# Kernel tuning notes

Hardware: AMD Instinct MI355X
Metric: run time of the kernel (lower is better)

The kernel has to match this reference:

```python
import jax, jax.numpy as jnp
import numpy as np

B, I, H, T = 65536, 64, 64, 16  # batch, input_size, hidden_size, type_num


def setup_inputs() -> dict:
    key = jax.random.key(0)
    ks = jax.random.split(key, 10)
    s = 0.1  # ~1/sqrt(H) init scale like torch GRUCell
    return {
        "x": jax.random.normal(ks[0], (B, I), jnp.float32),
        "typ": jax.random.randint(ks[1], (B,), 0, T, jnp.int32),
        "c": jax.random.normal(ks[2], (B, H), jnp.float32),
        "registers": jax.random.normal(ks[3], (B, T, H), jnp.float32),
        # per-type GRUCell bank (stacked across types)
        "Wih": jax.random.normal(ks[4], (T, 3 * H, I), jnp.float32) * s,
        "Whh": jax.random.normal(ks[5], (T, 3 * H, H), jnp.float32) * s,
        "bih": jax.random.normal(ks[6], (T, 3 * H), jnp.float32) * s,
        "bhh": jax.random.normal(ks[7], (T, 3 * H), jnp.float32) * s,
        # core GRUCell: input = flattened registers (T*H)
        "cWih": jax.random.normal(ks[8], (3 * H, T * H), jnp.float32) * s,
        "cWhh": jax.random.normal(ks[9], (3 * H, H), jnp.float32) * s,
        "cbih": jnp.zeros((3 * H,), jnp.float32),
        "cbhh": jnp.zeros((3 * H,), jnp.float32),
    }


def _gru(gi, gh, h):
    # torch.nn.GRUCell math; gi/gh: (..., 3H), h: (..., H)
    ir, iz, in_ = jnp.split(gi, 3, axis=-1)
    hr, hz, hn = jnp.split(gh, 3, axis=-1)
    r = jax.nn.sigmoid(ir + hr)
    z = jax.nn.sigmoid(iz + hz)
    n = jnp.tanh(in_ + r * hn)
    return (1.0 - z) * n + z * h


def reference(x, typ, c, registers, Wih, Whh, bih, bhh, cWih, cWhh, cbih, cbhh):
    # Bank of T GRUCells, all run on the same input x with per-type hidden = registers[:, t]
    gi = jnp.einsum('bi,tgi->btg', x, Wih) + bih[None]            # (B,T,3H)
    gh = jnp.einsum('bth,tgh->btg', registers, Whh) + bhh[None]   # (B,T,3H)
    hidden_tmp = _gru(gi, gh, registers)                          # (B,T,H)

    # Gather/scatter register update: only slot typ[b] takes its GRU output,
    # all other slots keep the old register (exactly what hidden_all[N, I] does).
    mask = (jnp.arange(T)[None, :] == typ[:, None])[..., None]    # (B,T,1)
    reg_new = jnp.where(mask, hidden_tmp, registers)              # (B,T,H)

    # core_v2: core GRUCell over flattened registers with state c
    xflat = reg_new.reshape(B, T * H)
    cgi = xflat @ cWih.T + cbih
    cgh = c @ cWhh.T + cbhh
    core = _gru(cgi, cgh, c)                                      # (B,H)
    return core
```

## Files before the change

kernel.cpp:

```cpp
#include <hip/hip_runtime.h>

typedef unsigned short u16;
typedef unsigned int u32;
typedef __bf16 bf16x8 __attribute__((ext_vector_type(8)));
typedef float f32x4 __attribute__((ext_vector_type(4)));
typedef u32 u32x2 __attribute__((ext_vector_type(2)));
typedef u32 u32x4 __attribute__((ext_vector_type(4)));


__device__ __forceinline__ u16 f2bf(float f) {
  union { float f; u32 u; } v; v.f = f;
  u32 u = v.u;
  u32 r = (u + 0x7fffu + ((u >> 16) & 1u)) >> 16;
  return (u16)r;
}
__device__ __forceinline__ float bf2f(u16 h) {
  union { u32 u; float f; } v; v.u = ((u32)h) << 16;
  return v.f;
}
__device__ __forceinline__ u32 pack2(float a, float b) {
  return (u32)f2bf(a) | ((u32)f2bf(b) << 16);
}
__device__ __forceinline__ float sigf(float x) { return 1.0f / (1.0f + __expf(-x)); }
__device__ __forceinline__ float tanh_fast(float x) { return 2.0f * sigf(2.0f * x) - 1.0f; }

__global__ __launch_bounds__(256) void k0_convert(
    const float* __restrict__ Wih, const float* __restrict__ Whh,
    const float* __restrict__ cWih, const float* __restrict__ cWhh,
    u16* __restrict__ wih_bf, u16* __restrict__ whh_bf,
    u16* __restrict__ cwih_bf, u16* __restrict__ cwhh_bf)
{
  int i = blockIdx.x * 256 + threadIdx.x;
  if (i < 196608) {
    wih_bf[i]  = f2bf(Wih[i]);
    whh_bf[i]  = f2bf(Whh[i]);
    cwih_bf[i] = f2bf(cWih[i]);
  }
  if (i < 12288) cwhh_bf[i] = f2bf(cWhh[i]);
}

__global__ __launch_bounds__(256) void k1_pertype(
    const float* __restrict__ x, const int* __restrict__ typ,
    const float* __restrict__ regs,
    const u16* __restrict__ wih_bf, const u16* __restrict__ whh_bf,
    const float* __restrict__ bih, const float* __restrict__ bhh,
    u16* __restrict__ hnew)
{
  const int t = blockIdx.y;
  const int base = blockIdx.x * 1024;
  const int tid = threadIdx.x;

  __shared__ int s_count;
  __shared__ int s_list[1024];
  __shared__ __align__(16) u16 sAx[16 * 72];
  __shared__ __align__(16) u16 sAh[16 * 72];

  if (tid == 0) s_count = 0;
  __syncthreads();
  for (int i = tid; i < 1024; i += 256) {
    if (typ[base + i] == t) {
      int p = atomicAdd(&s_count, 1);
      s_list[p] = base + i;
    }
  }
  __syncthreads();
  const int count = s_count;
  if (count == 0) return;

  const int lane = tid & 63;
  const int w = tid >> 6;
  const int col = lane & 15;
  const int quad = lane >> 4;
  const int hidx = w * 16 + col;

  bf16x8 bw[3][2], bh[3][2];
#pragma unroll
  for (int g = 0; g < 3; ++g) {
    const u16* pw = wih_bf + (t * 192 + g * 64 + hidx) * 64;
    const u16* ph = whh_bf + (t * 192 + g * 64 + hidx) * 64;
#pragma unroll
    for (int s = 0; s < 2; ++s) {
      bw[g][s] = *(const bf16x8*)(pw + s * 32 + quad * 8);
      bh[g][s] = *(const bf16x8*)(ph + s * 32 + quad * 8);
    }
  }
  float vbih[3], vbhh[3];
#pragma unroll
  for (int g = 0; g < 3; ++g) {
    vbih[g] = bih[t * 192 + g * 64 + hidx];
    vbhh[g] = bhh[t * 192 + g * 64 + hidx];
  }

  const int srow = tid >> 4;
  const int sk4 = (tid & 15) * 4;
  const f32x4 zero = {0.f, 0.f, 0.f, 0.f};

  for (int tile = 0; tile < count; tile += 16) {
    __syncthreads();
    {
      int r = tile + srow;
      int b = s_list[r < count ? r : count - 1];
      float4 vx = *(const float4*)(x + b * 64 + sk4);
      float4 vh = *(const float4*)(regs + (b * 16 + t) * 64 + sk4);
      u32x2 px, ph2;
      px[0] = pack2(vx.x, vx.y); px[1] = pack2(vx.z, vx.w);
      ph2[0] = pack2(vh.x, vh.y); ph2[1] = pack2(vh.z, vh.w);
      *(u32x2*)(&sAx[srow * 72 + sk4]) = px;
      *(u32x2*)(&sAh[srow * 72 + sk4]) = ph2;
    }
    __syncthreads();

    f32x4 agi[3], agh[3];
#pragma unroll
    for (int g = 0; g < 3; ++g) { agi[g] = zero; agh[g] = zero; }
#pragma unroll
    for (int s = 0; s < 2; ++s) {
      bf16x8 ax = *(const bf16x8*)(&sAx[col * 72 + s * 32 + quad * 8]);
      bf16x8 ah = *(const bf16x8*)(&sAh[col * 72 + s * 32 + quad * 8]);
#pragma unroll
      for (int g = 0; g < 3; ++g) {
        agi[g] = __builtin_amdgcn_mfma_f32_16x16x32_bf16(ax, bw[g][s], agi[g], 0, 0, 0);
        agh[g] = __builtin_amdgcn_mfma_f32_16x16x32_bf16(ah, bh[g][s], agh[g], 0, 0, 0);
      }
    }
#pragma unroll
    for (int rr = 0; rr < 4; ++rr) {
      int m = quad * 4 + rr;
      int gr = tile + m;
      if (gr < count) {
        int b2 = s_list[gr];
        float ir  = agi[0][rr] + vbih[0];
        float iz  = agi[1][rr] + vbih[1];
        float in_ = agi[2][rr] + vbih[2];
        float hr  = agh[0][rr] + vbhh[0];
        float hz  = agh[1][rr] + vbhh[1];
        float hn  = agh[2][rr] + vbhh[2];
        float rg = sigf(ir + hr);
        float zg = sigf(iz + hz);
        float ng = tanh_fast(in_ + rg * hn);
        float hold = bf2f(sAh[m * 72 + hidx]);
        hnew[b2 * 64 + hidx] = f2bf((1.f - zg) * ng + zg * hold);
      }
    }
  }
}

__global__ __launch_bounds__(256) void k2_core(
    const float* __restrict__ regs, const int* __restrict__ typ,
    const float* __restrict__ c, const u16* __restrict__ hnew,
    const u16* __restrict__ cwih_bf, const u16* __restrict__ cwhh_bf,
    const float* __restrict__ cbih, const float* __restrict__ cbhh,
    float* __restrict__ out)
{
  __shared__ __align__(16) u16 sA[64 * 72];
  __shared__ __align__(16) u16 sB[192 * 72];
  __shared__ int s_typ[64];

  const int tid = threadIdx.x;
  const int rowbase = blockIdx.x * 64;
  if (tid < 64) s_typ[tid] = typ[rowbase + tid];

  const int lane = tid & 63;
  const int w = tid >> 6;
  const int col = lane & 15;
  const int quad = lane >> 4;
  const f32x4 zero = {0.f, 0.f, 0.f, 0.f};

  f32x4 agi[4][3];
#pragma unroll
  for (int mt = 0; mt < 4; ++mt)
#pragma unroll
    for (int g = 0; g < 3; ++g) agi[mt][g] = zero;

  for (int s = 0; s < 16; ++s) {
    __syncthreads();
#pragma unroll
    for (int j = 0; j < 6; ++j) {
      int u = tid + 256 * j;
      int n = u >> 3, ko = (u & 7) * 8;
      *(u32x4*)(&sB[n * 72 + ko]) = *(const u32x4*)(cwih_bf + n * 1024 + s * 64 + ko);
    }
#pragma unroll
    for (int j = 0; j < 4; ++j) {
      int v = tid + 256 * j;
      int row = v >> 4, k4 = (v & 15) * 4;
      int b = rowbase + row;
      if (s_typ[row] == s) {
        *(u32x2*)(&sA[row * 72 + k4]) = *(const u32x2*)(hnew + b * 64 + k4);
      } else {
        float4 vv = *(const float4*)(regs + (b * 16 + s) * 64 + k4);
        u32x2 pp; pp[0] = pack2(vv.x, vv.y); pp[1] = pack2(vv.z, vv.w);
        *(u32x2*)(&sA[row * 72 + k4]) = pp;
      }
    }
    __syncthreads();
#pragma unroll
    for (int ks = 0; ks < 2; ++ks) {
      bf16x8 bfr[3];
#pragma unroll
      for (int g = 0; g < 3; ++g)
        bfr[g] = *(const bf16x8*)(&sB[(g * 64 + w * 16 + col) * 72 + ks * 32 + quad * 8]);
#pragma unroll
      for (int mt = 0; mt < 4; ++mt) {
        bf16x8 af = *(const bf16x8*)(&sA[(mt * 16 + col) * 72 + ks * 32 + quad * 8]);
#pragma unroll
        for (int g = 0; g < 3; ++g)
          agi[mt][g] = __builtin_amdgcn_mfma_f32_16x16x32_bf16(af, bfr[g], agi[mt][g], 0, 0, 0);
      }
    }
  }

  f32x4 agh[4][3];
#pragma unroll
  for (int mt = 0; mt < 4; ++mt)
#pragma unroll
    for (int g = 0; g < 3; ++g) agh[mt][g] = zero;

  __syncthreads();
#pragma unroll
  for (int j = 0; j < 6; ++j) {
    int u = tid + 256 * j;
    int n = u >> 3, ko = (u & 7) * 8;
    *(u32x4*)(&sB[n * 72 + ko]) = *(const u32x4*)(cwhh_bf + n * 64 + ko);
  }
#pragma unroll
  for (int j = 0; j < 4; ++j) {
    int v = tid + 256 * j;
    int row = v >> 4, k4 = (v & 15) * 4;
    int b = rowbase + row;
    float4 vv = *(const float4*)(c + b * 64 + k4);
    u32x2 pp; pp[0] = pack2(vv.x, vv.y); pp[1] = pack2(vv.z, vv.w);
    *(u32x2*)(&sA[row * 72 + k4]) = pp;
  }
  __syncthreads();
#pragma unroll
  for (int ks = 0; ks < 2; ++ks) {
    bf16x8 bfr[3];
#pragma unroll
    for (int g = 0; g < 3; ++g)
      bfr[g] = *(const bf16x8*)(&sB[(g * 64 + w * 16 + col) * 72 + ks * 32 + quad * 8]);
#pragma unroll
    for (int mt = 0; mt < 4; ++mt) {
      bf16x8 af = *(const bf16x8*)(&sA[(mt * 16 + col) * 72 + ks * 32 + quad * 8]);
#pragma unroll
      for (int g = 0; g < 3; ++g)
        agh[mt][g] = __builtin_amdgcn_mfma_f32_16x16x32_bf16(af, bfr[g], agh[mt][g], 0, 0, 0);
    }
  }

  const int hidx = w * 16 + col;
  float b0 = cbih[hidx], b1 = cbih[64 + hidx], b2 = cbih[128 + hidx];
  float d0 = cbhh[hidx], d1 = cbhh[64 + hidx], d2 = cbhh[128 + hidx];
#pragma unroll
  for (int mt = 0; mt < 4; ++mt) {
#pragma unroll
    for (int rr = 0; rr < 4; ++rr) {
      int row = mt * 16 + quad * 4 + rr;
      int b = rowbase + row;
      float ir  = agi[mt][0][rr] + b0;
      float iz  = agi[mt][1][rr] + b1;
      float in_ = agi[mt][2][rr] + b2;
      float hr  = agh[mt][0][rr] + d0;
      float hz  = agh[mt][1][rr] + d1;
      float hn  = agh[mt][2][rr] + d2;
      float rg = sigf(ir + hr);
      float zg = sigf(iz + hz);
      float ng = tanh_fast(in_ + rg * hn);
      float cold = c[b * 64 + hidx];
      out[b * 64 + hidx] = (1.f - zg) * ng + zg * cold;
    }
  }
}

extern "C" void kernel_launch(void* const* d_in, const int* in_sizes, int n_in,
                              void* d_out, int out_size, void* d_ws, size_t ws_size,
                              hipStream_t stream) {
  const float* x    = (const float*)d_in[0];
  const int*   typ  = (const int*)d_in[1];
  const float* c    = (const float*)d_in[2];
  const float* regs = (const float*)d_in[3];
  const float* Wih  = (const float*)d_in[4];
  const float* Whh  = (const float*)d_in[5];
  const float* bih  = (const float*)d_in[6];
  const float* bhh  = (const float*)d_in[7];
  const float* cWih = (const float*)d_in[8];
  const float* cWhh = (const float*)d_in[9];
  const float* cbih = (const float*)d_in[10];
  const float* cbhh = (const float*)d_in[11];
  float* out = (float*)d_out;

  char* ws = (char*)d_ws;
  u16* hnew    = (u16*)ws;
  u16* wih_bf  = (u16*)(ws + (size_t)8 * 1024 * 1024);
  u16* whh_bf  = wih_bf + 196608;
  u16* cwih_bf = whh_bf + 196608;
  u16* cwhh_bf = cwih_bf + 196608;

  k0_convert<<<768, 256, 0, stream>>>(Wih, Whh, cWih, cWhh, wih_bf, whh_bf, cwih_bf, cwhh_bf);
  k1_pertype<<<dim3(64, 16), 256, 0, stream>>>(x, typ, regs, wih_bf, whh_bf, bih, bhh, hnew);
  k2_core<<<1024, 256, 0, stream>>>(regs, typ, c, hnew, cwih_bf, cwhh_bf, cbih, cbhh, out);
}
```

Before: 543.8 us.

## Fuse per-type GRU and core GRU into one kernel with LDS-resident registers

Merges the per-type GRU kernel and the core GRU kernel into a single kernel. Each 64-row block loads its full register slab once into LDS as bf16, sorts rows by type, and computes the per-type GRU outputs into LDS. The core GEMM then reads from LDS, with weights streamed straight from global into registers and prefetched one step ahead. This removes the hnew round-trip and the second read of the registers, at the cost of about 133KB of LDS per block, which limits occupancy to one block per CU.

```diff
diff --git a/kernel.cpp b/kernel.cpp
--- a/kernel.cpp
+++ b/kernel.cpp
@@ -5,14 +5,12 @@
 typedef __bf16 bf16x8 __attribute__((ext_vector_type(8)));
 typedef float f32x4 __attribute__((ext_vector_type(4)));
 typedef u32 u32x2 __attribute__((ext_vector_type(2)));
-typedef u32 u32x4 __attribute__((ext_vector_type(4)));
 
 
 __device__ __forceinline__ u16 f2bf(float f) {
   union { float f; u32 u; } v; v.f = f;
   u32 u = v.u;
-  u32 r = (u + 0x7fffu + ((u >> 16) & 1u)) >> 16;
-  return (u16)r;
+  return (u16)((u + 0x7fffu + ((u >> 16) & 1u)) >> 16);
 }
 __device__ __forceinline__ float bf2f(u16 h) {
   union { u32 u; float f; } v; v.u = ((u32)h) << 16;
@@ -20,6 +18,12 @@
 }
 __device__ __forceinline__ u32 pack2(float a, float b) {
   return (u32)f2bf(a) | ((u32)f2bf(b) << 16);
+}
+__device__ __forceinline__ bf16x8 pack8(float4 a, float4 b) {
+  union { u32 u[4]; bf16x8 v; } r;
+  r.u[0] = pack2(a.x, a.y); r.u[1] = pack2(a.z, a.w);
+  r.u[2] = pack2(b.x, b.y); r.u[3] = pack2(b.z, b.w);
+  return r.v;
 }
 __device__ __forceinline__ float sigf(float x) { return 1.0f / (1.0f + __expf(-x)); }
 __device__ __forceinline__ float tanh_fast(float x) { return 2.0f * sigf(2.0f * x) - 1.0f; }
@@ -39,132 +43,164 @@
   if (i < 12288) cwhh_bf[i] = f2bf(cWhh[i]);
 }
 
-__global__ __launch_bounds__(256) void k1_pertype(
+#define SA 1040
+#define SH 72
+
+__global__ __launch_bounds__(256) void kf_fused(
     const float* __restrict__ x, const int* __restrict__ typ,
-    const float* __restrict__ regs,
+    const float* __restrict__ c, const float* __restrict__ regs,
     const u16* __restrict__ wih_bf, const u16* __restrict__ whh_bf,
     const float* __restrict__ bih, const float* __restrict__ bhh,
-    u16* __restrict__ hnew)
+    const u16* __restrict__ cwih_bf, const u16* __restrict__ cwhh_bf,
+    const float* __restrict__ cbih, const float* __restrict__ cbhh,
+    float* __restrict__ out)
 {
-  const int t = blockIdx.y;
-  const int base = blockIdx.x * 1024;
+  __shared__ __align__(16) u16 sA[64 * SA];
+  __shared__ __align__(16) u16 sH[64 * SH];
+  __shared__ int s_typ[64];
+  __shared__ int s_order[64];
+  __shared__ int s_cnt[16], s_off[16], s_cnt2[16];
+  __shared__ int s_gt[24], s_gs[24], s_ge[24];
+  __shared__ int s_ng;
+
   const int tid = threadIdx.x;
-
-  __shared__ int s_count;
-  __shared__ int s_list[1024];
-  __shared__ __align__(16) u16 sAx[16 * 72];
-  __shared__ __align__(16) u16 sAh[16 * 72];
-
-  if (tid == 0) s_count = 0;
-  __syncthreads();
-  for (int i = tid; i < 1024; i += 256) {
-    if (typ[base + i] == t) {
-      int p = atomicAdd(&s_count, 1);
-      s_list[p] = base + i;
-    }
-  }
-  __syncthreads();
-  const int count = s_count;
-  if (count == 0) return;
-
+  const int b0 = blockIdx.x * 64;
   const int lane = tid & 63;
   const int w = tid >> 6;
   const int col = lane & 15;
   const int quad = lane >> 4;
   const int hidx = w * 16 + col;
-
-  bf16x8 bw[3][2], bh[3][2];
-#pragma unroll
-  for (int g = 0; g < 3; ++g) {
-    const u16* pw = wih_bf + (t * 192 + g * 64 + hidx) * 64;
-    const u16* ph = whh_bf + (t * 192 + g * 64 + hidx) * 64;
-#pragma unroll
-    for (int s = 0; s < 2; ++s) {
-      bw[g][s] = *(const bf16x8*)(pw + s * 32 + quad * 8);
-      bh[g][s] = *(const bf16x8*)(ph + s * 32 + quad * 8);
-    }
-  }
-  float vbih[3], vbhh[3];
-#pragma unroll
-  for (int g = 0; g < 3; ++g) {
-    vbih[g] = bih[t * 192 + g * 64 + hidx];
-    vbhh[g] = bhh[t * 192 + g * 64 + hidx];
-  }
-
-  const int srow = tid >> 4;
-  const int sk4 = (tid & 15) * 4;
   const f32x4 zero = {0.f, 0.f, 0.f, 0.f};
 
-  for (int tile = 0; tile < count; tile += 16) {
-    __syncthreads();
-    {
-      int r = tile + srow;
-      int b = s_list[r < count ? r : count - 1];
-      float4 vx = *(const float4*)(x + b * 64 + sk4);
-      float4 vh = *(const float4*)(regs + (b * 16 + t) * 64 + sk4);
-      u32x2 px, ph2;
-      px[0] = pack2(vx.x, vx.y); px[1] = pack2(vx.z, vx.w);
-      ph2[0] = pack2(vh.x, vh.y); ph2[1] = pack2(vh.z, vh.w);
-      *(u32x2*)(&sAx[srow * 72 + sk4]) = px;
-      *(u32x2*)(&sAh[srow * 72 + sk4]) = ph2;
-    }
-    __syncthreads();
-
+  {
+    const float* src = regs + (size_t)b0 * 1024;
+    for (int j0 = 0; j0 < 64; j0 += 8) {
+      float4 v[8];
+#pragma unroll
+      for (int j = 0; j < 8; ++j)
+        v[j] = *(const float4*)(src + (size_t)(j0 + j) * 1024 + tid * 4);
+#pragma unroll
+      for (int j = 0; j < 8; ++j) {
+        u32x2 p; p[0] = pack2(v[j].x, v[j].y); p[1] = pack2(v[j].z, v[j].w);
+        *(u32x2*)(&sA[(j0 + j) * SA + tid * 4]) = p;
+      }
+    }
+  }
+
+  if (tid < 16) { s_cnt[tid] = 0; s_cnt2[tid] = 0; }
+  __syncthreads();
+  if (tid < 64) {
+    int t = typ[b0 + tid];
+    s_typ[tid] = t;
+    atomicAdd(&s_cnt[t], 1);
+  }
+  __syncthreads();
+  if (tid == 0) {
+    int off = 0, ng = 0;
+    for (int t = 0; t < 16; ++t) {
+      s_off[t] = off;
+      int cnt = s_cnt[t];
+      for (int base = 0; base < cnt; base += 16) {
+        s_gt[ng] = t; s_gs[ng] = off + base; s_ge[ng] = off + cnt; ++ng;
+      }
+      off += cnt;
+    }
+    s_ng = ng;
+  }
+  __syncthreads();
+  if (tid < 64) {
+    int t = s_typ[tid];
+    int p = s_off[t] + atomicAdd(&s_cnt2[t], 1);
+    s_order[p] = tid;
+  }
+  __syncthreads();
+
+  const int ng = s_ng;
+  for (int gi = 0; gi < ng; ++gi) {
+    const int t = s_gt[gi], gs = s_gs[gi], ge = s_ge[gi];
+    int p = gs + col;
+    int rowm = s_order[p < ge ? p : ge - 1];
+
+    bf16x8 bw[3][2], bh[3][2];
+#pragma unroll
+    for (int g = 0; g < 3; ++g) {
+      const u16* pw = wih_bf + (t * 192 + g * 64 + hidx) * 64;
+      const u16* ph = whh_bf + (t * 192 + g * 64 + hidx) * 64;
+#pragma unroll
+      for (int ks = 0; ks < 2; ++ks) {
+        bw[g][ks] = *(const bf16x8*)(pw + ks * 32 + quad * 8);
+        bh[g][ks] = *(const bf16x8*)(ph + ks * 32 + quad * 8);
+      }
+    }
+    bf16x8 ax[2], ah[2];
+#pragma unroll
+    for (int ks = 0; ks < 2; ++ks) {
+      const float* xr = x + (size_t)(b0 + rowm) * 64 + ks * 32 + quad * 8;
+      ax[ks] = pack8(*(const float4*)xr, *(const float4*)(xr + 4));
+      ah[ks] = *(const bf16x8*)(&sA[rowm * SA + t * 64 + ks * 32 + quad * 8]);
+    }
     f32x4 agi[3], agh[3];
 #pragma unroll
     for (int g = 0; g < 3; ++g) { agi[g] = zero; agh[g] = zero; }
 #pragma unroll
-    for (int s = 0; s < 2; ++s) {
-      bf16x8 ax = *(const bf16x8*)(&sAx[col * 72 + s * 32 + quad * 8]);
-      bf16x8 ah = *(const bf16x8*)(&sAh[col * 72 + s * 32 + quad * 8]);
+    for (int ks = 0; ks < 2; ++ks)
 #pragma unroll
       for (int g = 0; g < 3; ++g) {
-        agi[g] = __builtin_amdgcn_mfma_f32_16x16x32_bf16(ax, bw[g][s], agi[g], 0, 0, 0);
-        agh[g] = __builtin_amdgcn_mfma_f32_16x16x32_bf16(ah, bh[g][s], agh[g], 0, 0, 0);
-      }
+        agi[g] = __builtin_amdgcn_mfma_f32_16x16x32_bf16(ax[ks], bw[g][ks], agi[g], 0, 0, 0);
+        agh[g] = __builtin_amdgcn_mfma_f32_16x16x32_bf16(ah[ks], bh[g][ks], agh[g], 0, 0, 0);
+      }
+    float vbi[3], vbh[3];
+#pragma unroll
+    for (int g = 0; g < 3; ++g) {
+      vbi[g] = bih[t * 192 + g * 64 + hidx];
+      vbh[g] = bhh[t * 192 + g * 64 + hidx];
     }
 #pragma unroll
     for (int rr = 0; rr < 4; ++rr) {
-      int m = quad * 4 + rr;
-      int gr = tile + m;
-      if (gr < count) {
-        int b2 = s_list[gr];
-        float ir  = agi[0][rr] + vbih[0];
-        float iz  = agi[1][rr] + vbih[1];
-        float in_ = agi[2][rr] + vbih[2];
-        float hr  = agh[0][rr] + vbhh[0];
-        float hz  = agh[1][rr] + vbhh[1];
-        float hn  = agh[2][rr] + vbhh[2];
+      int pp = gs + quad * 4 + rr;
+      if (pp < ge) {
+        int r64 = s_order[pp];
+        float ir  = agi[0][rr] + vbi[0];
+        float iz  = agi[1][rr] + vbi[1];
+        float in_ = agi[2][rr] + vbi[2];
+        float hr  = agh[0][rr] + vbh[0];
+        float hz  = agh[1][rr] + vbh[1];
+        float hn  = agh[2][rr] + vbh[2];
         float rg = sigf(ir + hr);
         float zg = sigf(iz + hz);
-        float ng = tanh_fast(in_ + rg * hn);
-        float hold = bf2f(sAh[m * 72 + hidx]);
-        hnew[b2 * 64 + hidx] = f2bf((1.f - zg) * ng + zg * hold);
-      }
-    }
-  }
-}
-
-__global__ __launch_bounds__(256) void k2_core(
-    const float* __restrict__ regs, const int* __restrict__ typ,
-    const float* __restrict__ c, const u16* __restrict__ hnew,
-    const u16* __restrict__ cwih_bf, const u16* __restrict__ cwhh_bf,
-    const float* __restrict__ cbih, const float* __restrict__ cbhh,
-    float* __restrict__ out)
-{
-  __shared__ __align__(16) u16 sA[64 * 72];
-  __shared__ __align__(16) u16 sB[192 * 72];
-  __shared__ int s_typ[64];
-
-  const int tid = threadIdx.x;
-  const int rowbase = blockIdx.x * 64;
-  if (tid < 64) s_typ[tid] = typ[rowbase + tid];
-
-  const int lane = tid & 63;
-  const int w = tid >> 6;
-  const int col = lane & 15;
-  const int quad = lane >> 4;
-  const f32x4 zero = {0.f, 0.f, 0.f, 0.f};
+        float ngate = tanh_fast(in_ + rg * hn);
+        float hold = bf2f(sA[r64 * SA + t * 64 + hidx]);
+        sH[r64 * SH + hidx] = f2bf((1.f - zg) * ngate + zg * hold);
+      }
+    }
+  }
+  __syncthreads();
+
+  f32x4 agh[4][3];
+#pragma unroll
+  for (int mt = 0; mt < 4; ++mt)
+#pragma unroll
+    for (int g = 0; g < 3; ++g) agh[mt][g] = zero;
+
+  {
+    bf16x8 bh2[3][2];
+#pragma unroll
+    for (int g = 0; g < 3; ++g)
+#pragma unroll
+      for (int ks = 0; ks < 2; ++ks)
+        bh2[g][ks] = *(const bf16x8*)(cwhh_bf + (g * 64 + hidx) * 64 + ks * 32 + quad * 8);
+#pragma unroll
+    for (int mt = 0; mt < 4; ++mt) {
+#pragma unroll
+      for (int ks = 0; ks < 2; ++ks) {
+        const float* cr = c + (size_t)(b0 + mt * 16 + col) * 64 + ks * 32 + quad * 8;
+        bf16x8 af = pack8(*(const float4*)cr, *(const float4*)(cr + 4));
+#pragma unroll
+        for (int g = 0; g < 3; ++g)
+          agh[mt][g] = __builtin_amdgcn_mfma_f32_16x16x32_bf16(af, bh2[g][ks], agh[mt][g], 0, 0, 0);
+      }
+    }
+  }
 
   f32x4 agi[4][3];
 #pragma unroll
@@ -172,102 +208,63 @@
 #pragma unroll
     for (int g = 0; g < 3; ++g) agi[mt][g] = zero;
 
+  int rowtyp[4];
+#pragma unroll
+  for (int mt = 0; mt < 4; ++mt) rowtyp[mt] = s_typ[mt * 16 + col];
+
+  bf16x8 bnx[6];
+#pragma unroll
+  for (int g = 0; g < 3; ++g)
+#pragma unroll
+    for (int ks = 0; ks < 2; ++ks)
+      bnx[g * 2 + ks] = *(const bf16x8*)(cwih_bf + (g * 64 + hidx) * 1024 + ks * 32 + quad * 8);
+
   for (int s = 0; s < 16; ++s) {
-    __syncthreads();
-#pragma unroll
-    for (int j = 0; j < 6; ++j) {
-      int u = tid + 256 * j;
-      int n = u >> 3, ko = (u & 7) * 8;
-      *(u32x4*)(&sB[n * 72 + ko]) = *(const u32x4*)(cwih_bf + n * 1024 + s * 64 + ko);
-    }
-#pragma unroll
-    for (int j = 0; j < 4; ++j) {
-      int v = tid + 256 * j;
-      int row = v >> 4, k4 = (v & 15) * 4;
-      int b = rowbase + row;
-      if (s_typ[row] == s) {
-        *(u32x2*)(&sA[row * 72 + k4]) = *(const u32x2*)(hnew + b * 64 + k4);
-      } else {
-        float4 vv = *(const float4*)(regs + (b * 16 + s) * 64 + k4);
-        u32x2 pp; pp[0] = pack2(vv.x, vv.y); pp[1] = pack2(vv.z, vv.w);
-        *(u32x2*)(&sA[row * 72 + k4]) = pp;
-      }
-    }
-    __syncthreads();
+    bf16x8 bcur[6];
+#pragma unroll
+    for (int q = 0; q < 6; ++q) bcur[q] = bnx[q];
+    if (s + 1 < 16) {
+#pragma unroll
+      for (int g = 0; g < 3; ++g)
+#pragma unroll
+        for (int ks = 0; ks < 2; ++ks)
+          bnx[g * 2 + ks] = *(const bf16x8*)(cwih_bf + (g * 64 + hidx) * 1024 + (s + 1) * 64 + ks * 32 + quad * 8);
+    }
 #pragma unroll
     for (int ks = 0; ks < 2; ++ks) {
-      bf16x8 bfr[3];
-#pragma unroll
-      for (int g = 0; g < 3; ++g)
-        bfr[g] = *(const bf16x8*)(&sB[(g * 64 + w * 16 + col) * 72 + ks * 32 + quad * 8]);
 #pragma unroll
       for (int mt = 0; mt < 4; ++mt) {
-        bf16x8 af = *(const bf16x8*)(&sA[(mt * 16 + col) * 72 + ks * 32 + quad * 8]);
+        const int row = mt * 16 + col;
+        const int koff = ks * 32 + quad * 8;
+        const u16* src = (rowtyp[mt] == s) ? &sH[row * SH + koff]
+                                           : &sA[row * SA + s * 64 + koff];
+        bf16x8 af = *(const bf16x8*)src;
 #pragma unroll
         for (int g = 0; g < 3; ++g)
-          agi[mt][g] = __builtin_amdgcn_mfma_f32_16x16x32_bf16(af, bfr[g], agi[mt][g], 0, 0, 0);
-      }
-    }
-  }
-
-  f32x4 agh[4][3];
-#pragma unroll
-  for (int mt = 0; mt < 4; ++mt)
-#pragma unroll
-    for (int g = 0; g < 3; ++g) agh[mt][g] = zero;
-
-  __syncthreads();
-#pragma unroll
-  for (int j = 0; j < 6; ++j) {
-    int u = tid + 256 * j;
-    int n = u >> 3, ko = (u & 7) * 8;
-    *(u32x4*)(&sB[n * 72 + ko]) = *(const u32x4*)(cwhh_bf + n * 64 + ko);
-  }
-#pragma unroll
-  for (int j = 0; j < 4; ++j) {
-    int v = tid + 256 * j;
-    int row = v >> 4, k4 = (v & 15) * 4;
-    int b = rowbase + row;
-    float4 vv = *(const float4*)(c + b * 64 + k4);
-    u32x2 pp; pp[0] = pack2(vv.x, vv.y); pp[1] = pack2(vv.z, vv.w);
-    *(u32x2*)(&sA[row * 72 + k4]) = pp;
-  }
-  __syncthreads();
-#pragma unroll
-  for (int ks = 0; ks < 2; ++ks) {
-    bf16x8 bfr[3];
-#pragma unroll
-    for (int g = 0; g < 3; ++g)
-      bfr[g] = *(const bf16x8*)(&sB[(g * 64 + w * 16 + col) * 72 + ks * 32 + quad * 8]);
-#pragma unroll
-    for (int mt = 0; mt < 4; ++mt) {
-      bf16x8 af = *(const bf16x8*)(&sA[(mt * 16 + col) * 72 + ks * 32 + quad * 8]);
-#pragma unroll
-      for (int g = 0; g < 3; ++g)
-        agh[mt][g] = __builtin_amdgcn_mfma_f32_16x16x32_bf16(af, bfr[g], agh[mt][g], 0, 0, 0);
-    }
-  }
-
-  const int hidx = w * 16 + col;
-  float b0 = cbih[hidx], b1 = cbih[64 + hidx], b2 = cbih[128 + hidx];
+          agi[mt][g] = __builtin_amdgcn_mfma_f32_16x16x32_bf16(af, bcur[g * 2 + ks], agi[mt][g], 0, 0, 0);
+      }
+    }
+  }
+
+  float e0 = cbih[hidx], e1 = cbih[64 + hidx], e2 = cbih[128 + hidx];
   float d0 = cbhh[hidx], d1 = cbhh[64 + hidx], d2 = cbhh[128 + hidx];
 #pragma unroll
   for (int mt = 0; mt < 4; ++mt) {
 #pragma unroll
     for (int rr = 0; rr < 4; ++rr) {
       int row = mt * 16 + quad * 4 + rr;
-      int b = rowbase + row;
-      float ir  = agi[mt][0][rr] + b0;
-      float iz  = agi[mt][1][rr] + b1;
-      float in_ = agi[mt][2][rr] + b2;
+      int b = b0 + row;
+      float ir  = agi[mt][0][rr] + e0;
+      float iz  = agi[mt][1][rr] + e1;
+      float in_ = agi[mt][2][rr] + e2;
       float hr  = agh[mt][0][rr] + d0;
       float hz  = agh[mt][1][rr] + d1;
       float hn  = agh[mt][2][rr] + d2;
       float rg = sigf(ir + hr);
       float zg = sigf(iz + hz);
-      float ng = tanh_fast(in_ + rg * hn);
-      float cold = c[b * 64 + hidx];
-      out[b * 64 + hidx] = (1.f - zg) * ng + zg * cold;
+      float ngate = tanh_fast(in_ + rg * hn);
+      float cold = c[(size_t)b * 64 + hidx];
+      out[(size_t)b * 64 + hidx] = (1.f - zg) * ngate + zg * cold;
     }
   }
 }
@@ -289,14 +286,12 @@
   const float* cbhh = (const float*)d_in[11];
   float* out = (float*)d_out;
 
-  char* ws = (char*)d_ws;
-  u16* hnew    = (u16*)ws;
-  u16* wih_bf  = (u16*)(ws + (size_t)8 * 1024 * 1024);
+  u16* wih_bf  = (u16*)d_ws;
   u16* whh_bf  = wih_bf + 196608;
   u16* cwih_bf = whh_bf + 196608;
   u16* cwhh_bf = cwih_bf + 196608;
 
   k0_convert<<<768, 256, 0, stream>>>(Wih, Whh, cWih, cWhh, wih_bf, whh_bf, cwih_bf, cwhh_bf);
-  k1_pertype<<<dim3(64, 16), 256, 0, stream>>>(x, typ, regs, wih_bf, whh_bf, bih, bhh, hnew);
-  k2_core<<<1024, 256, 0, stream>>>(regs, typ, c, hnew, cwih_bf, cwhh_bf, cbih, cbhh, out);
-}
+  kf_fused<<<1024, 256, 0, stream>>>(x, typ, c, regs, wih_bf, whh_bf, bih, bhh,
+                                     cwih_bf, cwhh_bf, cbih, cbhh, out);
+}
```

New measurement: 618.5 us. +13.7%, slower.
